# Optimization experiments

Measured on AMD Instinct MI355X. Metric: run time of the kernel, lower is better.

The kernel has to match this reference:

```python
import jax, jax.numpy as jnp
import numpy as np
from jax import lax

SUBSTEPS = 10
MACRO_DT = 1.0
MICRO_DT = MACRO_DT / float(SUBSTEPS)
MAX_DAYS = 4  # matches fill_max of delta_t_days; inactive batch items are masked to zero update


def _laplacian3d(u):
    # u: [B, 1, D, H, W]; 6-point stencil with zero (Dirichlet) padding at the boundary
    up = jnp.pad(u, ((0, 0), (0, 0), (1, 1), (1, 1), (1, 1)))
    return (up[:, :, 2:, 1:-1, 1:-1] + up[:, :, :-2, 1:-1, 1:-1]
            + up[:, :, 1:-1, 2:, 1:-1] + up[:, :, 1:-1, :-2, 1:-1]
            + up[:, :, 1:-1, 1:-1, 2:] + up[:, :, 1:-1, 1:-1, :-2]
            - 6.0 * u)


def _fisher_kolmogorov(u, D_map, rho_map):
    # du/dt = D * laplacian(u) + rho * u * (1 - u)
    return D_map * _laplacian3d(u) + rho_map * u * (1.0 - u)


def setup_inputs() -> dict:
    key = jax.random.key(0)
    k1, k2, k3, k4 = jax.random.split(key, 4)
    shape = (2, 1, 128, 128, 128)
    u_t0 = jax.random.uniform(k1, shape, dtype=jnp.float32)
    D_map = jax.random.uniform(k2, shape, dtype=jnp.float32) * 0.1   # diffusion, keep CFL-stable
    rho_map = jax.random.uniform(k3, shape, dtype=jnp.float32) * 0.5  # proliferation rate
    delta_t_days = jax.random.randint(k4, (2,), 0, MAX_DAYS, dtype=jnp.int32)
    return {"u_t0": u_t0, "D_map": D_map, "rho_map": rho_map, "delta_t_days": delta_t_days}


def reference(u_t0, D_map, rho_map, delta_t_days):
    # Sequential explicit-Euler rollout with per-batch-item active masking.
    days = jnp.arange(MAX_DAYS * SUBSTEPS, dtype=jnp.int32) // SUBSTEPS  # macro day of each micro-step

    def micro_step(u, day):
        active = (day < delta_t_days).astype(u.dtype)[:, None, None, None, None]  # [B,1,1,1,1]
        du_dt = _fisher_kolmogorov(u, D_map, rho_map)
        return u + active * MICRO_DT * du_dt, None

    u_final, _ = lax.scan(micro_step, u_t0, days)
    return jnp.clip(u_final, 0.0, 1.0)
```

## Files before the change

kernel.cpp:

```cpp
#include <hip/hip_runtime.h>
#include <cstdint>


constexpr int NX = 128, NY = 128, NZ = 128;
constexpr int PLANE = NX * NY;
constexpr int VOL   = NZ * PLANE;
constexpr int TOTAL = 2 * VOL;
constexpr float DT  = 0.1f;
constexpr int MAX_PAIRS = 20;

constexpr int TY = 8, TZ = 4;
constexpr int RY = TY + 2, RZ = TZ + 2;
constexpr int REGION_F4 = RZ * RY * 32;
constexpr int BLOCKS = 2 * (NZ / TZ) * (NY / TY);

__device__ __forceinline__ float4 ld4(const float* p) { return *(const float4*)p; }

__device__ __forceinline__ uint32_t f2bf(float f) {
    uint32_t u = __float_as_uint(f);
    u += 0x7fffu + ((u >> 16) & 1u);
    return u >> 16;
}
__device__ __forceinline__ float bf_lo(uint32_t p) { return __uint_as_float(p << 16); }
__device__ __forceinline__ float bf_hi(uint32_t p) { return __uint_as_float(p & 0xffff0000u); }
__device__ __forceinline__ float clip01(float v) { return fminf(fmaxf(v, 0.0f), 1.0f); }

__device__ __forceinline__ float4 fkstep(float4 c, float xm, float xp,
                                         float4 ym, float4 yp,
                                         float4 zm, float4 zp,
                                         float4 Dv, float4 Rv) {
    float4 o;
    o.x = fmaf(DT, fmaf(Dv.x, (xm + c.y) + (ym.x + yp.x) + (zm.x + zp.x) - 6.0f * c.x,
                        Rv.x * c.x * (1.0f - c.x)), c.x);
    o.y = fmaf(DT, fmaf(Dv.y, (c.x + c.z) + (ym.y + yp.y) + (zm.y + zp.y) - 6.0f * c.y,
                        Rv.y * c.y * (1.0f - c.y)), c.y);
    o.z = fmaf(DT, fmaf(Dv.z, (c.y + c.w) + (ym.z + yp.z) + (zm.z + zp.z) - 6.0f * c.z,
                        Rv.z * c.z * (1.0f - c.z)), c.z);
    o.w = fmaf(DT, fmaf(Dv.w, (c.z + xp) + (ym.w + yp.w) + (zm.w + zp.w) - 6.0f * c.w,
                        Rv.w * c.w * (1.0f - c.w)), c.w);
    return o;
}

__global__ __launch_bounds__(256, 4)
void fk_pair(const float* __restrict__ src, float* __restrict__ dst0,
             float* __restrict__ out, const float* __restrict__ u0,
             const float* __restrict__ Dm, const float* __restrict__ Rm,
             uint32_t* __restrict__ dr, const int* __restrict__ dtd, int p)
{
    const int b  = blockIdx.x >> 9;
    int d = dtd[b]; d = d < 0 ? 0 : (d > 4 ? 4 : d);
    const int steps = d * 10;

    const int zb = (blockIdx.x >> 4) & 31;
    const int yt = blockIdx.x & 15;
    const int z0 = zb * TZ, y0 = yt * TY;
    const int tid = threadIdx.x;
    const int xq  = tid & 31;
    const int yi  = tid >> 5;
    const int baseb = b << 21;
    const float4 zero = make_float4(0.f, 0.f, 0.f, 0.f);

    if (2 * p >= steps) {
        if (steps == 0 && p == 0) {
            #pragma unroll
            for (int k = 0; k < TZ; ++k) {
                const int idx = baseb + (z0 + k) * PLANE + (y0 + yi) * NX + (xq << 2);
                const float4 v = ld4(u0 + idx);
                float4 o;
                o.x = clip01(v.x); o.y = clip01(v.y);
                o.z = clip01(v.z); o.w = clip01(v.w);
                *(float4*)(out + idx) = o;
            }
        }
        return;
    }
    const bool first = (p == 0);
    const bool last  = (2 * p == steps - 2);
    float* __restrict__ dst = last ? out : dst0;

    __shared__ float s1[RZ * RY * NX];

    #pragma unroll 2
    for (int it = 0; it < 8; ++it) {
        const int i = tid + it * 256;
        if (i >= REGION_F4) break;
        const int cxq = i & 31;
        const int t2  = i >> 5;
        const int ry  = t2 % RY;
        const int rz  = t2 / RY;
        const int y = y0 - 1 + ry;
        const int z = z0 - 1 + rz;
        float4 o = zero;
        if ((unsigned)y < (unsigned)NY && (unsigned)z < (unsigned)NZ) {
            const int idx = baseb + z * PLANE + y * NX + (cxq << 2);
            const float4 c  = ld4(src + idx);
            const float xm  = (cxq > 0)  ? src[idx - 1] : 0.0f;
            const float xp  = (cxq < 31) ? src[idx + 4] : 0.0f;
            const float4 ym4 = (y > 0)      ? ld4(src + idx - NX)    : zero;
            const float4 yp4 = (y < NY - 1) ? ld4(src + idx + NX)    : zero;
            const float4 zm4 = (z > 0)      ? ld4(src + idx - PLANE) : zero;
            const float4 zp4 = (z < NZ - 1) ? ld4(src + idx + PLANE) : zero;
            float4 Dv, Rv;
            if (first) {
                Dv = ld4(Dm + idx);
                Rv = ld4(Rm + idx);
            } else {
                const uint4 pr = *(const uint4*)(dr + idx);
                Dv.x = bf_lo(pr.x); Dv.y = bf_lo(pr.y); Dv.z = bf_lo(pr.z); Dv.w = bf_lo(pr.w);
                Rv.x = bf_hi(pr.x); Rv.y = bf_hi(pr.y); Rv.z = bf_hi(pr.z); Rv.w = bf_hi(pr.w);
            }
            o = fkstep(c, xm, xp, ym4, yp4, zm4, zp4, Dv, Rv);
        }
        *(float4*)&s1[t2 * NX + (cxq << 2)] = o;
    }
    __syncthreads();

    const int ry = yi + 1;
    const int y  = y0 + yi;
    #pragma unroll
    for (int k = 0; k < TZ; ++k) {
        const int rz = k + 1;
        const float* rowc = &s1[(rz * RY + ry) * NX];
        const float4 c = *(const float4*)&rowc[xq << 2];
        float xm = 0.0f, xp = 0.0f;
        if (xq > 0)  xm = ((const float4*)&rowc[(xq - 1) << 2])->w;
        if (xq < 31) xp = ((const float4*)&rowc[(xq + 1) << 2])->x;
        const float4 ym4 = *(const float4*)&s1[(rz * RY + ry - 1) * NX + (xq << 2)];
        const float4 yp4 = *(const float4*)&s1[(rz * RY + ry + 1) * NX + (xq << 2)];
        const float4 zm4 = *(const float4*)&s1[((rz - 1) * RY + ry) * NX + (xq << 2)];
        const float4 zp4 = *(const float4*)&s1[((rz + 1) * RY + ry) * NX + (xq << 2)];

        const int idx = baseb + (z0 + k) * PLANE + y * NX + (xq << 2);
        float4 Dv, Rv;
        if (first) {
            Dv = ld4(Dm + idx);
            Rv = ld4(Rm + idx);
            uint4 pk;
            pk.x = f2bf(Dv.x) | (f2bf(Rv.x) << 16);
            pk.y = f2bf(Dv.y) | (f2bf(Rv.y) << 16);
            pk.z = f2bf(Dv.z) | (f2bf(Rv.z) << 16);
            pk.w = f2bf(Dv.w) | (f2bf(Rv.w) << 16);
            *(uint4*)(dr + idx) = pk;
        } else {
            const uint4 pr = *(const uint4*)(dr + idx);
            Dv.x = bf_lo(pr.x); Dv.y = bf_lo(pr.y); Dv.z = bf_lo(pr.z); Dv.w = bf_lo(pr.w);
            Rv.x = bf_hi(pr.x); Rv.y = bf_hi(pr.y); Rv.z = bf_hi(pr.z); Rv.w = bf_hi(pr.w);
        }
        float4 o = fkstep(c, xm, xp, ym4, yp4, zm4, zp4, Dv, Rv);
        if (last) {
            o.x = clip01(o.x); o.y = clip01(o.y);
            o.z = clip01(o.z); o.w = clip01(o.w);
        }
        *(float4*)(dst + idx) = o;
    }
}

extern "C" void kernel_launch(void* const* d_in, const int* in_sizes, int n_in,
                              void* d_out, int out_size, void* d_ws, size_t ws_size,
                              hipStream_t stream) {
    const float* u0  = (const float*)d_in[0];
    const float* Dm  = (const float*)d_in[1];
    const float* Rm  = (const float*)d_in[2];
    const int*   dtd = (const int*)d_in[3];
    float* out = (float*)d_out;
    float* ws  = (float*)d_ws;
    float* buf[2] = { ws, ws + TOTAL };
    uint32_t* dr = (uint32_t*)(ws + 2 * TOTAL);

    for (int p = 0; p < MAX_PAIRS; ++p) {
        const float* src = (p == 0) ? u0 : buf[(p - 1) & 1];
        fk_pair<<<BLOCKS, 256, 0, stream>>>(src, buf[p & 1], out, u0,
                                            Dm, Rm, dr, dtd, p);
    }
}
```

Before: 248.0 us.

## Enlarge z tile, register-march interior with cached D/rho pack, halo-only ring

The z tile grows from 4 to 8 planes. Each thread now computes the first substep for its own interior column by marching along z in registers, reusing the previous and current planes instead of reloading them. A separate loop computes only the halo ring cells. The packed bf16 D/rho values read for the interior are kept in registers and reused for the second substep, which avoids a second global read. The aim is to cut redundant halo recompute and global traffic per pair. In exchange, the launch-bounds occupancy target drops from 4 to 2, register pressure rises and the grid has half as many blocks.

Measured after the change: 289.0 us. 16.5% more time.

```diff
diff --git a/kernel.cpp b/kernel.cpp
--- a/kernel.cpp
+++ b/kernel.cpp
@@ -9,9 +9,10 @@
 constexpr float DT  = 0.1f;
 constexpr int MAX_PAIRS = 20;
 
-constexpr int TY = 8, TZ = 4;
+constexpr int TY = 8, TZ = 8;
 constexpr int RY = TY + 2, RZ = TZ + 2;
-constexpr int REGION_F4 = RZ * RY * 32;
+constexpr int RING_ROWS = RZ * RY - TZ * TY;
+constexpr int RING_F4   = RING_ROWS * 32;
 constexpr int BLOCKS = 2 * (NZ / TZ) * (NY / TY);
 
 __device__ __forceinline__ float4 ld4(const float* p) { return *(const float4*)p; }
@@ -41,17 +42,24 @@
     return o;
 }
 
-__global__ __launch_bounds__(256, 4)
+__device__ __forceinline__ float4 unpackD(uint4 p) {
+    return make_float4(bf_lo(p.x), bf_lo(p.y), bf_lo(p.z), bf_lo(p.w));
+}
+__device__ __forceinline__ float4 unpackR(uint4 p) {
+    return make_float4(bf_hi(p.x), bf_hi(p.y), bf_hi(p.z), bf_hi(p.w));
+}
+
+__global__ __launch_bounds__(256, 2)
 void fk_pair(const float* __restrict__ src, float* __restrict__ dst0,
              float* __restrict__ out, const float* __restrict__ u0,
              const float* __restrict__ Dm, const float* __restrict__ Rm,
              uint32_t* __restrict__ dr, const int* __restrict__ dtd, int p)
 {
-    const int b  = blockIdx.x >> 9;
+    const int b  = blockIdx.x >> 8;
     int d = dtd[b]; d = d < 0 ? 0 : (d > 4 ? 4 : d);
     const int steps = d * 10;
 
-    const int zb = (blockIdx.x >> 4) & 31;
+    const int zb = (blockIdx.x >> 4) & 15;
     const int yt = blockIdx.x & 15;
     const int z0 = zb * TZ, y0 = yt * TY;
     const int tid = threadIdx.x;
@@ -80,14 +88,53 @@
 
     __shared__ float s1[RZ * RY * NX];
 
-    #pragma unroll 2
-    for (int it = 0; it < 8; ++it) {
-        const int i = tid + it * 256;
-        if (i >= REGION_F4) break;
+    uint4 pr[TZ];
+    {
+        const int y = y0 + yi;
+        const int colbase = baseb + y * NX + (xq << 2);
+        const bool has_ym = (y > 0), has_yp = (y < NY - 1);
+        const bool has_l = (xq > 0), has_r = (xq < 31);
+
+        float4 um = (z0 > 0) ? ld4(src + colbase + (z0 - 1) * PLANE) : zero;
+        float4 uc = ld4(src + colbase + z0 * PLANE);
+        #pragma unroll
+        for (int k = 0; k < TZ; ++k) {
+            const int z = z0 + k;
+            const int idx = colbase + z * PLANE;
+            const float4 un = (z < NZ - 1) ? ld4(src + idx + PLANE) : zero;
+            const float4 ym4 = has_ym ? ld4(src + idx - NX) : zero;
+            const float4 yp4 = has_yp ? ld4(src + idx + NX) : zero;
+            const float xm = has_l ? src[idx - 1] : 0.0f;
+            const float xp = has_r ? src[idx + 4] : 0.0f;
+            float4 Dv, Rv;
+            if (first) {
+                Dv = ld4(Dm + idx);
+                Rv = ld4(Rm + idx);
+                uint4 pk;
+                pk.x = f2bf(Dv.x) | (f2bf(Rv.x) << 16);
+                pk.y = f2bf(Dv.y) | (f2bf(Rv.y) << 16);
+                pk.z = f2bf(Dv.z) | (f2bf(Rv.z) << 16);
+                pk.w = f2bf(Dv.w) | (f2bf(Rv.w) << 16);
+                *(uint4*)(dr + idx) = pk;
+                pr[k] = pk;
+            } else {
+                pr[k] = *(const uint4*)(dr + idx);
+                Dv = unpackD(pr[k]);
+                Rv = unpackR(pr[k]);
+            }
+            const float4 o = fkstep(uc, xm, xp, ym4, yp4, um, un, Dv, Rv);
+            *(float4*)&s1[((k + 1) * RY + (yi + 1)) * NX + (xq << 2)] = o;
+            um = uc; uc = un;
+        }
+    }
+
+    for (int i = tid; i < RING_F4; i += 256) {
         const int cxq = i & 31;
-        const int t2  = i >> 5;
-        const int ry  = t2 % RY;
-        const int rz  = t2 / RY;
+        const int r   = i >> 5;
+        int rz, ry;
+        if (r < 10)      { rz = 0; ry = r; }
+        else if (r < 20) { rz = 9; ry = r - 10; }
+        else { const int q = r - 20; rz = 1 + (q >> 1); ry = (q & 1) ? 9 : 0; }
         const int y = y0 - 1 + ry;
         const int z = z0 - 1 + rz;
         float4 o = zero;
@@ -105,53 +152,42 @@
                 Dv = ld4(Dm + idx);
                 Rv = ld4(Rm + idx);
             } else {
-                const uint4 pr = *(const uint4*)(dr + idx);
-                Dv.x = bf_lo(pr.x); Dv.y = bf_lo(pr.y); Dv.z = bf_lo(pr.z); Dv.w = bf_lo(pr.w);
-                Rv.x = bf_hi(pr.x); Rv.y = bf_hi(pr.y); Rv.z = bf_hi(pr.z); Rv.w = bf_hi(pr.w);
+                const uint4 pk = *(const uint4*)(dr + idx);
+                Dv = unpackD(pk);
+                Rv = unpackR(pk);
             }
             o = fkstep(c, xm, xp, ym4, yp4, zm4, zp4, Dv, Rv);
         }
-        *(float4*)&s1[t2 * NX + (cxq << 2)] = o;
+        *(float4*)&s1[(rz * RY + ry) * NX + (cxq << 2)] = o;
     }
     __syncthreads();
 
-    const int ry = yi + 1;
-    const int y  = y0 + yi;
-    #pragma unroll
-    for (int k = 0; k < TZ; ++k) {
-        const int rz = k + 1;
-        const float* rowc = &s1[(rz * RY + ry) * NX];
-        const float4 c = *(const float4*)&rowc[xq << 2];
-        float xm = 0.0f, xp = 0.0f;
-        if (xq > 0)  xm = ((const float4*)&rowc[(xq - 1) << 2])->w;
-        if (xq < 31) xp = ((const float4*)&rowc[(xq + 1) << 2])->x;
-        const float4 ym4 = *(const float4*)&s1[(rz * RY + ry - 1) * NX + (xq << 2)];
-        const float4 yp4 = *(const float4*)&s1[(rz * RY + ry + 1) * NX + (xq << 2)];
-        const float4 zm4 = *(const float4*)&s1[((rz - 1) * RY + ry) * NX + (xq << 2)];
-        const float4 zp4 = *(const float4*)&s1[((rz + 1) * RY + ry) * NX + (xq << 2)];
-
-        const int idx = baseb + (z0 + k) * PLANE + y * NX + (xq << 2);
-        float4 Dv, Rv;
-        if (first) {
-            Dv = ld4(Dm + idx);
-            Rv = ld4(Rm + idx);
-            uint4 pk;
-            pk.x = f2bf(Dv.x) | (f2bf(Rv.x) << 16);
-            pk.y = f2bf(Dv.y) | (f2bf(Rv.y) << 16);
-            pk.z = f2bf(Dv.z) | (f2bf(Rv.z) << 16);
-            pk.w = f2bf(Dv.w) | (f2bf(Rv.w) << 16);
-            *(uint4*)(dr + idx) = pk;
-        } else {
-            const uint4 pr = *(const uint4*)(dr + idx);
-            Dv.x = bf_lo(pr.x); Dv.y = bf_lo(pr.y); Dv.z = bf_lo(pr.z); Dv.w = bf_lo(pr.w);
-            Rv.x = bf_hi(pr.x); Rv.y = bf_hi(pr.y); Rv.z = bf_hi(pr.z); Rv.w = bf_hi(pr.w);
-        }
-        float4 o = fkstep(c, xm, xp, ym4, yp4, zm4, zp4, Dv, Rv);
-        if (last) {
-            o.x = clip01(o.x); o.y = clip01(o.y);
-            o.z = clip01(o.z); o.w = clip01(o.w);
-        }
-        *(float4*)(dst + idx) = o;
+    {
+        const int ry = yi + 1;
+        const int y  = y0 + yi;
+        float4 zmv = *(const float4*)&s1[(0 * RY + ry) * NX + (xq << 2)];
+        float4 cv  = *(const float4*)&s1[(1 * RY + ry) * NX + (xq << 2)];
+        #pragma unroll
+        for (int k = 0; k < TZ; ++k) {
+            const int rz = k + 1;
+            const float4 zpv = *(const float4*)&s1[((rz + 1) * RY + ry) * NX + (xq << 2)];
+            const float* rowc = &s1[(rz * RY + ry) * NX];
+            float xm = 0.0f, xp = 0.0f;
+            if (xq > 0)  xm = ((const float4*)&rowc[(xq - 1) << 2])->w;
+            if (xq < 31) xp = ((const float4*)&rowc[(xq + 1) << 2])->x;
+            const float4 ym4 = *(const float4*)&s1[(rz * RY + ry - 1) * NX + (xq << 2)];
+            const float4 yp4 = *(const float4*)&s1[(rz * RY + ry + 1) * NX + (xq << 2)];
+
+            float4 o = fkstep(cv, xm, xp, ym4, yp4, zmv, zpv,
+                              unpackD(pr[k]), unpackR(pr[k]));
+            if (last) {
+                o.x = clip01(o.x); o.y = clip01(o.y);
+                o.z = clip01(o.z); o.w = clip01(o.w);
+            }
+            const int idx = baseb + (z0 + k) * PLANE + y * NX + (xq << 2);
+            *(float4*)(dst + idx) = o;
+            zmv = cv; cv = zpv;
+        }
     }
 }
 
```
